# Performance work log

Hardware: AMD Instinct MI355X
Metric: run time of the kernel (lower is better)

Reference implementation:

```python
import jax, jax.numpy as jnp
import numpy as np

B, T, C = 4, 2048, 1024
H = 16
DH = C // H  # 64


def setup_inputs() -> dict:
    key = jax.random.key(0)
    ks = jax.random.split(key, 10)
    s_in = 1.0 / np.sqrt(C)
    x = jax.random.normal(ks[0], (B, T, C), dtype=jnp.float32)
    # stacked per-head projection weights: [H, C, DH]
    Wq = jax.random.normal(ks[1], (H, C, DH), dtype=jnp.float32) * s_in
    bq = jnp.zeros((H, DH), dtype=jnp.float32)
    Wk = jax.random.normal(ks[2], (H, C, DH), dtype=jnp.float32) * s_in
    bk = jnp.zeros((H, DH), dtype=jnp.float32)
    Wv = jax.random.normal(ks[3], (H, C, DH), dtype=jnp.float32) * s_in
    bv = jnp.zeros((H, DH), dtype=jnp.float32)
    Wo = jax.random.normal(ks[4], (C, C), dtype=jnp.float32) * s_in
    bo = jnp.zeros((C,), dtype=jnp.float32)
    return {"x": x, "Wq": Wq, "bq": bq, "Wk": Wk, "bk": bk,
            "Wv": Wv, "bv": bv, "Wo": Wo, "bo": bo}


def reference(x, Wq, bq, Wk, bk, Wv, bv, Wo, bo):
    # per-head projections: (B,T,C) x (H,C,DH) -> (B,H,T,DH)
    q = jnp.einsum('btc,hcd->bhtd', x, Wq) + bq[None, :, None, :]
    k = jnp.einsum('btc,hcd->bhtd', x, Wk) + bk[None, :, None, :]
    v = jnp.einsum('btc,hcd->bhtd', x, Wv) + bv[None, :, None, :]
    # scores scaled by C**-0.5 (C = full input embedding dim, as in source)
    scale = jnp.float32(C) ** -0.5
    scores = jnp.einsum('bhtd,bhsd->bhts', q, k) * scale  # (B,H,T,T)
    causal = jnp.tril(jnp.ones((T, T), dtype=bool))
    scores = jnp.where(causal, scores, -jnp.inf)
    attn = jax.nn.softmax(scores, axis=-1)
    out = jnp.einsum('bhts,bhsd->bhtd', attn, v)  # (B,H,T,DH)
    out = out.transpose(0, 2, 1, 3).reshape(B, T, C)  # concat heads
    return out @ Wo + bo
```

## Files before the change

### kernel.cpp

```cpp
#include <hip/hip_runtime.h>
#include <hip/hip_bf16.h>

#define TDIM 2048
#define BDIM 4
#define CDIM 1024
#define HDIM 16
#define DH   64

typedef __hip_bfloat16 bf16;
typedef __attribute__((ext_vector_type(8))) short bf16x8;
typedef __attribute__((ext_vector_type(4))) short bf16x4;
typedef __attribute__((ext_vector_type(4))) float f32x4;

__device__ __forceinline__ void async_ld16(const bf16* g, bf16* l) {
    __builtin_amdgcn_global_load_lds(
        (const __attribute__((address_space(1))) unsigned int*)g,
        (__attribute__((address_space(3))) unsigned int*)l, 16, 0, 0);
}

__device__ __forceinline__ unsigned short bf16bits(float x) {
    bf16 b = __float2bfloat16(x);
    return *(unsigned short*)&b;
}

__device__ __forceinline__ float fast_exp2(float x) {
#if __has_builtin(__builtin_amdgcn_exp2f)
    return __builtin_amdgcn_exp2f(x);
#else
    return exp2f(x);
#endif
}

__device__ __forceinline__ f32x4 mfma_16x16x16_bf16(bf16x4 a, bf16x4 b, f32x4 c) {
#if __has_builtin(__builtin_amdgcn_mfma_f32_16x16x16_bf16)
    return __builtin_amdgcn_mfma_f32_16x16x16_bf16(a, b, c, 0, 0, 0);
#elif __has_builtin(__builtin_amdgcn_mfma_f32_16x16x16bf16_1k)
    return __builtin_amdgcn_mfma_f32_16x16x16bf16_1k(a, b, c, 0, 0, 0);
#else
    asm volatile("v_mfma_f32_16x16x16_bf16 %0, %1, %2, %0"
                 : "+v"(c) : "v"(a), "v"(b));
    return c;
#endif
}

__global__ void convert_x4(const float4* __restrict__ src, ushort4* __restrict__ dst, int n4) {
    int i = blockIdx.x * blockDim.x + threadIdx.x;
    if (i >= n4) return;
    float4 v = src[i];
    ushort4 o;
    o.x = bf16bits(v.x); o.y = bf16bits(v.y);
    o.z = bf16bits(v.z); o.w = bf16bits(v.w);
    dst[i] = o;
}

__global__ void convert_biases(const float* __restrict__ b0, const float* __restrict__ b1,
                               const float* __restrict__ b2, const float* __restrict__ b3,
                               bf16* __restrict__ dst) {
    int i = blockIdx.x * blockDim.x + threadIdx.x;
    int which = i >> 10, j = i & 1023;
    const float* src = (which == 0) ? b0 : (which == 1) ? b1 : (which == 2) ? b2 : b3;
    dst[i] = __float2bfloat16(src[j]);
}

__global__ __launch_bounds__(256) void transpose_qkv_kernel(
    const float* __restrict__ Wq, const float* __restrict__ Wk, const float* __restrict__ Wv,
    bf16* __restrict__ WqT, bf16* __restrict__ WkT, bf16* __restrict__ WvT) {
    __shared__ float tile[64][65];
    const int which = blockIdx.z >> 4, h = blockIdx.z & 15;
    const float* W  = ((which == 0) ? Wq  : (which == 1) ? Wk  : Wv)  + (size_t)h * CDIM * DH;
    bf16*        WT = ((which == 0) ? WqT : (which == 1) ? WkT : WvT) + (size_t)h * CDIM * DH;
    const int c0 = blockIdx.x * 64;
    for (int it = 0; it < 16; it++) {
        int e = it * 256 + threadIdx.x;
        int r = e >> 6, col = e & 63;
        tile[r][col] = W[(size_t)(c0 + r) * DH + col];
    }
    __syncthreads();
    for (int it = 0; it < 16; it++) {
        int e = it * 256 + threadIdx.x;
        int r = e >> 6, col = e & 63;
        WT[(size_t)r * CDIM + c0 + col] = __float2bfloat16(tile[col][r]);
    }
}

__global__ __launch_bounds__(256) void transpose_wo_kernel(
    const float* __restrict__ W, bf16* __restrict__ WT) {
    __shared__ float tile[64][65];
    const int c0 = blockIdx.x * 64, d0 = blockIdx.y * 64;
    for (int it = 0; it < 16; it++) {
        int e = it * 256 + threadIdx.x;
        int r = e >> 6, col = e & 63;
        tile[r][col] = W[(size_t)(c0 + r) * CDIM + d0 + col];
    }
    __syncthreads();
    for (int it = 0; it < 16; it++) {
        int e = it * 256 + threadIdx.x;
        int r = e >> 6, col = e & 63;
        WT[(size_t)(d0 + r) * CDIM + c0 + col] = __float2bfloat16(tile[col][r]);
    }
}

__global__ __launch_bounds__(256) void transpose_v_kernel(
    const bf16* __restrict__ V, bf16* __restrict__ Vt) {
    __shared__ unsigned short tile[64][65];
    const int bh = blockIdx.y, t0 = blockIdx.x * 64;
    const unsigned short* Vp  = (const unsigned short*)V + ((size_t)bh * TDIM + t0) * DH;
    unsigned short*       Vtp = (unsigned short*)Vt + (size_t)bh * DH * TDIM;
    for (int it = 0; it < 16; it++) {
        int e = it * 256 + threadIdx.x;
        int r = e >> 6, c = e & 63;
        tile[r][c] = Vp[(size_t)r * DH + c];
    }
    __syncthreads();
    for (int it = 0; it < 16; it++) {
        int e = it * 256 + threadIdx.x;
        int r = e >> 6, c = e & 63;
        Vtp[(size_t)r * TDIM + t0 + c] = tile[c][r];
    }
}

__global__ __launch_bounds__(256) void proj_qkv_kernel(
    const bf16* __restrict__ X,
    const bf16* __restrict__ WqT, const bf16* __restrict__ WkT, const bf16* __restrict__ WvT,
    const bf16* __restrict__ bq,  const bf16* __restrict__ bk,  const bf16* __restrict__ bvv,
    bf16* __restrict__ Qo, bf16* __restrict__ Ko, bf16* __restrict__ Vo)
{
    const int lin  = blockIdx.x + (int)gridDim.x * (blockIdx.y + (int)gridDim.y * blockIdx.z);
    const int xcd  = lin & 7;
    const int s    = lin >> 3;
    const int mloc = s & 7;
    const int rest = s >> 3;
    const int nblk = rest & 7;
    const int z    = rest >> 3;

    const bf16* Bt   = (z == 0) ? WqT : (z == 1) ? WkT : WvT;
    const bf16* bias = (z == 0) ? bq  : (z == 1) ? bk  : bvv;

    __shared__ __align__(16) bf16 As[128 * 32];
    __shared__ __align__(16) bf16 Bs[128 * 32];

    const int tid  = threadIdx.x;
    const int lane = tid & 63;
    const int wave = tid >> 6;
    const int wr = wave >> 1, wc = wave & 1;
    const int l15 = lane & 15, quad = lane >> 4;

    const int blockM = (xcd * 8 + mloc) * 128;
    const int blockN = nblk * 128;

    f32x4 acc[4][4];
    for (int i = 0; i < 4; i++)
        for (int j = 0; j < 4; j++)
            acc[i][j] = (f32x4){0.f, 0.f, 0.f, 0.f};

    const int srow = lane >> 2, scol = (lane & 3) * 8;
    for (int k0 = 0; k0 < CDIM; k0 += 32) {
        for (int cc = 0; cc < 2; cc++) {
            int chunk = wave * 2 + cc;
            int row = chunk * 16 + srow;
            async_ld16(&X [(size_t)(blockM + row) * CDIM + k0 + scol], &As[chunk * 512]);
            async_ld16(&Bt[(size_t)(blockN + row) * CDIM + k0 + scol], &Bs[chunk * 512]);
        }
        __syncthreads();

        bf16x8 af[4], bfr[4];
        for (int mi = 0; mi < 4; mi++)
            af[mi] = *(const bf16x8*)&As[(wr * 64 + mi * 16 + l15) * 32 + quad * 8];
        for (int ni = 0; ni < 4; ni++)
            bfr[ni] = *(const bf16x8*)&Bs[(wc * 64 + ni * 16 + l15) * 32 + quad * 8];

        for (int mi = 0; mi < 4; mi++)
            for (int ni = 0; ni < 4; ni++)
                acc[mi][ni] = __builtin_amdgcn_mfma_f32_16x16x32_bf16(
                    af[mi], bfr[ni], acc[mi][ni], 0, 0, 0);
        __syncthreads();
    }

    for (int mi = 0; mi < 4; mi++) {
        int mbase = blockM + wr * 64 + mi * 16 + quad * 4;
        for (int ni = 0; ni < 4; ni++) {
            int n = blockN + wc * 64 + ni * 16 + l15;
            float bval = __bfloat162float(bias[n]);
            int h = n >> 6, d = n & 63;
            for (int r = 0; r < 4; r++) {
                int mm = mbase + r;
                int b = mm >> 11, t = mm & 2047;
                float val = acc[mi][ni][r] + bval;
                size_t idx = (((size_t)b * HDIM + h) * TDIM + t) * DH + d;
                if (z == 0)      Qo[idx] = __float2bfloat16(val * 0.045084439f);
                else if (z == 1) Ko[idx] = __float2bfloat16(val);
                else             Vo[idx] = __float2bfloat16(val);
            }
        }
    }
}

__global__ __launch_bounds__(256) void proj_out_kernel(
    const bf16* __restrict__ X, const bf16* __restrict__ Bt,
    const bf16* __restrict__ bias, float* __restrict__ Out)
{
    const int lin  = blockIdx.x + (int)gridDim.x * blockIdx.y;
    const int xcd  = lin & 7;
    const int s    = lin >> 3;
    const int mloc = s & 7;
    const int nblk = s >> 3;

    __shared__ __align__(16) bf16 As[128 * 32];
    __shared__ __align__(16) bf16 Bs[128 * 32];

    const int tid  = threadIdx.x;
    const int lane = tid & 63;
    const int wave = tid >> 6;
    const int wr = wave >> 1, wc = wave & 1;
    const int l15 = lane & 15, quad = lane >> 4;

    const int blockM = (xcd * 8 + mloc) * 128;
    const int blockN = nblk * 128;

    f32x4 acc[4][4];
    for (int i = 0; i < 4; i++)
        for (int j = 0; j < 4; j++)
            acc[i][j] = (f32x4){0.f, 0.f, 0.f, 0.f};

    const int srow = lane >> 2, scol = (lane & 3) * 8;
    for (int k0 = 0; k0 < CDIM; k0 += 32) {
        for (int cc = 0; cc < 2; cc++) {
            int chunk = wave * 2 + cc;
            int row = chunk * 16 + srow;
            async_ld16(&X [(size_t)(blockM + row) * CDIM + k0 + scol], &As[chunk * 512]);
            async_ld16(&Bt[(size_t)(blockN + row) * CDIM + k0 + scol], &Bs[chunk * 512]);
        }
        __syncthreads();

        bf16x8 af[4], bfr[4];
        for (int mi = 0; mi < 4; mi++)
            af[mi] = *(const bf16x8*)&As[(wr * 64 + mi * 16 + l15) * 32 + quad * 8];
        for (int ni = 0; ni < 4; ni++)
            bfr[ni] = *(const bf16x8*)&Bs[(wc * 64 + ni * 16 + l15) * 32 + quad * 8];

        for (int mi = 0; mi < 4; mi++)
            for (int ni = 0; ni < 4; ni++)
                acc[mi][ni] = __builtin_amdgcn_mfma_f32_16x16x32_bf16(
                    af[mi], bfr[ni], acc[mi][ni], 0, 0, 0);
        __syncthreads();
    }

    for (int mi = 0; mi < 4; mi++) {
        int mbase = blockM + wr * 64 + mi * 16 + quad * 4;
        for (int ni = 0; ni < 4; ni++) {
            int n = blockN + wc * 64 + ni * 16 + l15;
            float bval = __bfloat162float(bias[n]);
            for (int r = 0; r < 4; r++)
                Out[(size_t)(mbase + r) * CDIM + n] = acc[mi][ni][r] + bval;
        }
    }
}

__global__ __launch_bounds__(256, 4) void attn_kernel(
    const bf16* __restrict__ Q, const bf16* __restrict__ Kb,
    const bf16* __restrict__ Vt, bf16* __restrict__ Y)
{
    const int lin  = blockIdx.x + (int)gridDim.x * blockIdx.y;
    const int slot = lin >> 3;
    const int bh   = (lin & 7) * 8 + (slot >> 4);
    const int qT   = 15 - (slot & 15);
    const int qBase = qT * 128;
    const int tid  = threadIdx.x;
    const int lane = tid & 63, wave = tid >> 6;
    const int l15 = lane & 15, quad = lane >> 4;

    __shared__ __align__(16) bf16 smem[2 * 2 * 64 * 64];

    bf16x8 qf[2][2];
    for (int g = 0; g < 2; g++) {
        const size_t qrow = (size_t)bh * TDIM + qBase + g * 64 + wave * 16 + l15;
        qf[g][0] = *(const bf16x8*)&Q[qrow * DH + quad * 8];
        qf[g][1] = *(const bf16x8*)&Q[qrow * DH + 32 + quad * 8];
    }

    f32x4 o[2][4];
    for (int g = 0; g < 2; g++)
        for (int mt = 0; mt < 4; mt++)
            o[g][mt] = (f32x4){0.f, 0.f, 0.f, 0.f};
    float lsum[2] = {0.f, 0.f};

    const int srow = (wave << 4) + (lane >> 3);
    const int ssc  = (((lane & 7) ^ (lane >> 3)) << 3);
    const bf16* kSrc0 = Kb + ((size_t)bh * TDIM + srow) * DH + ssc;
    const bf16* vSrc0 = Vt + ((size_t)bh * DH + srow) * TDIM + ssc;

    const int swA   = l15 & 7;
    const int kcol0 = ((quad ^ swA) << 3);
    const int kcol1 = (((4 + quad) ^ swA) << 3);
    const int u2    = quad >> 1, intra = ((quad & 1) << 2);

    const int nkt  = 2 * qT + 2;
    const int qloc = wave * 16 + l15;

    bf16* kD0 = smem + (wave * 16) * 64;
    bf16* vD0 = smem + 4096 + (wave * 16) * 64;

#define STAGE(tile, buf)                                            \
    do {                                                            \
        const bf16* kS_ = kSrc0 + (size_t)(tile) * 64 * DH;         \
        const bf16* vS_ = vSrc0 + (size_t)(tile) * 64;              \
        bf16* kD_ = kD0 + (buf) * 8192;                             \
        bf16* vD_ = vD0 + (buf) * 8192;                             \
        async_ld16(kS_,            kD_);                            \
        async_ld16(kS_ + 8 * DH,   kD_ + 8 * 64);                   \
        async_ld16(vS_,            vD_);                            \
        async_ld16(vS_ + 8 * TDIM, vD_ + 8 * 64);                   \
    } while (0)

    STAGE(0, 0);
    __syncthreads();

    int cur = 0;
    for (int kt = 0; kt < nkt; kt++) {
        if (kt + 1 < nkt) STAGE(kt + 1, cur ^ 1);
        const bf16* Ks = smem + cur * 8192;
        const bf16* Vs = Ks + 4096;

        const int dg = kt - 2 * qT;
        for (int nt = 0; nt < 4; nt++) {
            bf16x8 kf0 = *(const bf16x8*)&Ks[(nt * 16 + l15) * 64 + kcol0];
            bf16x8 kf1 = *(const bf16x8*)&Ks[(nt * 16 + l15) * 64 + kcol1];
            bf16x4 vA[4];
            for (int mt = 0; mt < 4; mt++)
                vA[mt] = *(const bf16x4*)&Vs[(mt * 16 + l15) * 64 +
                                             (((nt * 2 + u2) ^ swA) << 3) + intra];

            for (int g = 0; g < 2; g++) {
                if (dg == 1 && g == 0) continue;
                f32x4 s = (f32x4){0.f, 0.f, 0.f, 0.f};
                s = __builtin_amdgcn_mfma_f32_16x16x32_bf16(kf0, qf[g][0], s, 0, 0, 0);
                s = __builtin_amdgcn_mfma_f32_16x16x32_bf16(kf1, qf[g][1], s, 0, 0, 0);

                const bool diag = (dg == g);
                bf16x4 pb;
                for (int r = 0; r < 4; r++) {
                    float pe = fast_exp2(s[r]);
                    if (diag && (nt * 16 + quad * 4 + r > qloc)) pe = 0.f;
                    lsum[g] += pe;
                    pb[r] = (short)bf16bits(pe);
                }
                for (int mt = 0; mt < 4; mt++)
                    o[g][mt] = mfma_16x16x16_bf16(vA[mt], pb, o[g][mt]);
            }
        }
        __syncthreads();
        cur ^= 1;
    }
#undef STAGE

    const int b = bh >> 4, h = bh & 15;
    unsigned short* sm = (unsigned short*)smem;
    for (int g = 0; g < 2; g++) {
        float v = lsum[g];
        v += __shfl_xor(v, 16, 64);
        v += __shfl_xor(v, 32, 64);
        const float inv = 1.0f / v;

        for (int mt = 0; mt < 4; mt++) {
            unsigned short pk[4];
            for (int r = 0; r < 4; r++) pk[r] = bf16bits(o[g][mt][r] * inv);
            *(ushort4*)&sm[(wave * 16 + l15) * 72 + mt * 16 + quad * 4] = *(ushort4*)pk;
        }
        const int qq = lane >> 2, part = lane & 3;
        const int t = qBase + g * 64 + wave * 16 + qq;
        uint4 c0 = *(const uint4*)&sm[(wave * 16 + qq) * 72 + part * 16];
        uint4 c1 = *(const uint4*)&sm[(wave * 16 + qq) * 72 + part * 16 + 8];
        *(uint4*)&Y[((size_t)b * TDIM + t) * CDIM + h * DH + part * 16]     = c0;
        *(uint4*)&Y[((size_t)b * TDIM + t) * CDIM + h * DH + part * 16 + 8] = c1;
    }
}

extern "C" void kernel_launch(void* const* d_in, const int* in_sizes, int n_in,
                              void* d_out, int out_size, void* d_ws, size_t ws_size,
                              hipStream_t stream) {
    (void)in_sizes; (void)n_in; (void)out_size; (void)ws_size;

    char* ws = (char*)d_ws;
    const size_t SZ_BHTD = (size_t)BDIM * HDIM * TDIM * DH * sizeof(bf16);
    const size_t SZ_W    = (size_t)HDIM * CDIM * DH * sizeof(bf16);
    bf16* Qb  = (bf16*)(ws);
    bf16* Kb  = (bf16*)(ws + SZ_BHTD);
    bf16* Vt  = (bf16*)(ws + 2 * SZ_BHTD);
    bf16* Y   = (bf16*)(ws + 3 * SZ_BHTD);
    bf16* WqT = (bf16*)(ws + 4 * SZ_BHTD);
    bf16* WkT = (bf16*)(ws + 4 * SZ_BHTD + SZ_W);
    bf16* WvT = (bf16*)(ws + 4 * SZ_BHTD + 2 * SZ_W);
    bf16* WoT = (bf16*)(ws + 4 * SZ_BHTD + 3 * SZ_W);
    bf16* xC  = (bf16*)(ws + 4 * SZ_BHTD + 4 * SZ_W);
    bf16* bqC = (bf16*)(ws + 5 * SZ_BHTD + 4 * SZ_W);
    bf16* bkC = bqC + 1024;
    bf16* bvC = bqC + 2048;
    bf16* boC = bqC + 3072;
    bf16* Vb  = (bf16*)d_out;

    const int nX4 = (BDIM * TDIM * CDIM) / 4;
    convert_x4<<<nX4 / 256, 256, 0, stream>>>((const float4*)d_in[0], (ushort4*)xC, nX4);
    convert_biases<<<16, 256, 0, stream>>>((const float*)d_in[2], (const float*)d_in[4],
                                           (const float*)d_in[6], (const float*)d_in[8], bqC);

    transpose_qkv_kernel<<<dim3(CDIM / 64, 1, 48), 256, 0, stream>>>(
        (const float*)d_in[1], (const float*)d_in[3], (const float*)d_in[5], WqT, WkT, WvT);
    transpose_wo_kernel<<<dim3(CDIM / 64, CDIM / 64), 256, 0, stream>>>(
        (const float*)d_in[7], WoT);

    dim3 gq(CDIM / 128, (BDIM * TDIM) / 128, 3);
    proj_qkv_kernel<<<gq, 256, 0, stream>>>(xC, WqT, WkT, WvT, bqC, bkC, bvC, Qb, Kb, Vb);

    transpose_v_kernel<<<dim3(TDIM / 64, BDIM * HDIM), 256, 0, stream>>>(Vb, Vt);

    attn_kernel<<<dim3(TDIM / 128, BDIM * HDIM), 256, 0, stream>>>(Qb, Kb, Vt, Y);

    proj_out_kernel<<<dim3(CDIM / 128, (BDIM * TDIM) / 128), 256, 0, stream>>>(
        Y, WoT, boC, (float*)d_out);
}
```

Baseline: 280.4 us.

## Double-buffer GEMM LDS tiles and write V transposed from projection epilogue

Both projection GEMMs now use two LDS buffers, so the async global-to-LDS load for the next K tile is issued before the MFMAs on the current tile. This overlaps memory latency with compute and drops one barrier per iteration. The QKV projection epilogue writes V directly in transposed [b,h,d,t] layout with 4-element packed stores, which removes the separate transpose_v kernel and its round trip through global memory. The cost is twice the shared memory per block, which may lower occupancy.

```diff
diff --git a/kernel.cpp b/kernel.cpp
--- a/kernel.cpp
+++ b/kernel.cpp
@@ -100,30 +100,11 @@
     }
 }
 
-__global__ __launch_bounds__(256) void transpose_v_kernel(
-    const bf16* __restrict__ V, bf16* __restrict__ Vt) {
-    __shared__ unsigned short tile[64][65];
-    const int bh = blockIdx.y, t0 = blockIdx.x * 64;
-    const unsigned short* Vp  = (const unsigned short*)V + ((size_t)bh * TDIM + t0) * DH;
-    unsigned short*       Vtp = (unsigned short*)Vt + (size_t)bh * DH * TDIM;
-    for (int it = 0; it < 16; it++) {
-        int e = it * 256 + threadIdx.x;
-        int r = e >> 6, c = e & 63;
-        tile[r][c] = Vp[(size_t)r * DH + c];
-    }
-    __syncthreads();
-    for (int it = 0; it < 16; it++) {
-        int e = it * 256 + threadIdx.x;
-        int r = e >> 6, c = e & 63;
-        Vtp[(size_t)r * TDIM + t0 + c] = tile[c][r];
-    }
-}
-
 __global__ __launch_bounds__(256) void proj_qkv_kernel(
     const bf16* __restrict__ X,
     const bf16* __restrict__ WqT, const bf16* __restrict__ WkT, const bf16* __restrict__ WvT,
     const bf16* __restrict__ bq,  const bf16* __restrict__ bk,  const bf16* __restrict__ bvv,
-    bf16* __restrict__ Qo, bf16* __restrict__ Ko, bf16* __restrict__ Vo)
+    bf16* __restrict__ Qo, bf16* __restrict__ Ko, bf16* __restrict__ Vt)
 {
     const int lin  = blockIdx.x + (int)gridDim.x * (blockIdx.y + (int)gridDim.y * blockIdx.z);
     const int xcd  = lin & 7;
@@ -136,8 +117,8 @@
     const bf16* Bt   = (z == 0) ? WqT : (z == 1) ? WkT : WvT;
     const bf16* bias = (z == 0) ? bq  : (z == 1) ? bk  : bvv;
 
-    __shared__ __align__(16) bf16 As[128 * 32];
-    __shared__ __align__(16) bf16 Bs[128 * 32];
+    __shared__ __align__(16) bf16 As[2 * 128 * 32];
+    __shared__ __align__(16) bf16 Bs[2 * 128 * 32];
 
     const int tid  = threadIdx.x;
     const int lane = tid & 63;
@@ -154,42 +135,60 @@
             acc[i][j] = (f32x4){0.f, 0.f, 0.f, 0.f};
 
     const int srow = lane >> 2, scol = (lane & 3) * 8;
-    for (int k0 = 0; k0 < CDIM; k0 += 32) {
-        for (int cc = 0; cc < 2; cc++) {
-            int chunk = wave * 2 + cc;
-            int row = chunk * 16 + srow;
-            async_ld16(&X [(size_t)(blockM + row) * CDIM + k0 + scol], &As[chunk * 512]);
-            async_ld16(&Bt[(size_t)(blockN + row) * CDIM + k0 + scol], &Bs[chunk * 512]);
-        }
-        __syncthreads();
-
+#define PSTAGE(k0, buf)                                                          \
+    do {                                                                         \
+        for (int cc = 0; cc < 2; cc++) {                                         \
+            int chunk = wave * 2 + cc;                                           \
+            int row = chunk * 16 + srow;                                         \
+            async_ld16(&X [(size_t)(blockM + row) * CDIM + (k0) + scol],         \
+                       &As[(buf) * 4096 + chunk * 512]);                         \
+            async_ld16(&Bt[(size_t)(blockN + row) * CDIM + (k0) + scol],         \
+                       &Bs[(buf) * 4096 + chunk * 512]);                         \
+        }                                                                        \
+    } while (0)
+
+    PSTAGE(0, 0);
+    __syncthreads();
+
+    int cur = 0;
+    for (int kt = 0; kt < 32; kt++) {
+        if (kt + 1 < 32) PSTAGE((kt + 1) * 32, cur ^ 1);
+
+        const bf16* Ap = As + cur * 4096;
+        const bf16* Bp = Bs + cur * 4096;
         bf16x8 af[4], bfr[4];
         for (int mi = 0; mi < 4; mi++)
-            af[mi] = *(const bf16x8*)&As[(wr * 64 + mi * 16 + l15) * 32 + quad * 8];
+            af[mi] = *(const bf16x8*)&Ap[(wr * 64 + mi * 16 + l15) * 32 + quad * 8];
         for (int ni = 0; ni < 4; ni++)
-            bfr[ni] = *(const bf16x8*)&Bs[(wc * 64 + ni * 16 + l15) * 32 + quad * 8];
+            bfr[ni] = *(const bf16x8*)&Bp[(wc * 64 + ni * 16 + l15) * 32 + quad * 8];
 
         for (int mi = 0; mi < 4; mi++)
             for (int ni = 0; ni < 4; ni++)
                 acc[mi][ni] = __builtin_amdgcn_mfma_f32_16x16x32_bf16(
                     af[mi], bfr[ni], acc[mi][ni], 0, 0, 0);
         __syncthreads();
-    }
+        cur ^= 1;
+    }
+#undef PSTAGE
 
     for (int mi = 0; mi < 4; mi++) {
         int mbase = blockM + wr * 64 + mi * 16 + quad * 4;
+        int b = mbase >> 11, t = mbase & 2047;
         for (int ni = 0; ni < 4; ni++) {
             int n = blockN + wc * 64 + ni * 16 + l15;
             float bval = __bfloat162float(bias[n]);
             int h = n >> 6, d = n & 63;
-            for (int r = 0; r < 4; r++) {
-                int mm = mbase + r;
-                int b = mm >> 11, t = mm & 2047;
-                float val = acc[mi][ni][r] + bval;
-                size_t idx = (((size_t)b * HDIM + h) * TDIM + t) * DH + d;
-                if (z == 0)      Qo[idx] = __float2bfloat16(val * 0.045084439f);
-                else if (z == 1) Ko[idx] = __float2bfloat16(val);
-                else             Vo[idx] = __float2bfloat16(val);
+            if (z == 2) {
+                unsigned short pk[4];
+                for (int r = 0; r < 4; r++) pk[r] = bf16bits(acc[mi][ni][r] + bval);
+                *(ushort4*)&Vt[(((size_t)b * HDIM + h) * DH + d) * TDIM + t] = *(ushort4*)pk;
+            } else {
+                for (int r = 0; r < 4; r++) {
+                    float val = acc[mi][ni][r] + bval;
+                    size_t idx = (((size_t)b * HDIM + h) * TDIM + (t + r)) * DH + d;
+                    if (z == 0) Qo[idx] = __float2bfloat16(val * 0.045084439f);
+                    else        Ko[idx] = __float2bfloat16(val);
+                }
             }
         }
     }
@@ -205,8 +204,8 @@
     const int mloc = s & 7;
     const int nblk = s >> 3;
 
-    __shared__ __align__(16) bf16 As[128 * 32];
-    __shared__ __align__(16) bf16 Bs[128 * 32];
+    __shared__ __align__(16) bf16 As[2 * 128 * 32];
+    __shared__ __align__(16) bf16 Bs[2 * 128 * 32];
 
     const int tid  = threadIdx.x;
     const int lane = tid & 63;
@@ -223,27 +222,41 @@
             acc[i][j] = (f32x4){0.f, 0.f, 0.f, 0.f};
 
     const int srow = lane >> 2, scol = (lane & 3) * 8;
-    for (int k0 = 0; k0 < CDIM; k0 += 32) {
-        for (int cc = 0; cc < 2; cc++) {
-            int chunk = wave * 2 + cc;
-            int row = chunk * 16 + srow;
-            async_ld16(&X [(size_t)(blockM + row) * CDIM + k0 + scol], &As[chunk * 512]);
-            async_ld16(&Bt[(size_t)(blockN + row) * CDIM + k0 + scol], &Bs[chunk * 512]);
-        }
-        __syncthreads();
-
+#define PSTAGE(k0, buf)                                                          \
+    do {                                                                         \
+        for (int cc = 0; cc < 2; cc++) {                                         \
+            int chunk = wave * 2 + cc;                                           \
+            int row = chunk * 16 + srow;                                         \
+            async_ld16(&X [(size_t)(blockM + row) * CDIM + (k0) + scol],         \
+                       &As[(buf) * 4096 + chunk * 512]);                         \
+            async_ld16(&Bt[(size_t)(blockN + row) * CDIM + (k0) + scol],         \
+                       &Bs[(buf) * 4096 + chunk * 512]);                         \
+        }                                                                        \
+    } while (0)
+
+    PSTAGE(0, 0);
+    __syncthreads();
+
+    int cur = 0;
+    for (int kt = 0; kt < 32; kt++) {
+        if (kt + 1 < 32) PSTAGE((kt + 1) * 32, cur ^ 1);
+
+        const bf16* Ap = As + cur * 4096;
+        const bf16* Bp = Bs + cur * 4096;
         bf16x8 af[4], bfr[4];
         for (int mi = 0; mi < 4; mi++)
-            af[mi] = *(const bf16x8*)&As[(wr * 64 + mi * 16 + l15) * 32 + quad * 8];
+            af[mi] = *(const bf16x8*)&Ap[(wr * 64 + mi * 16 + l15) * 32 + quad * 8];
         for (int ni = 0; ni < 4; ni++)
-            bfr[ni] = *(const bf16x8*)&Bs[(wc * 64 + ni * 16 + l15) * 32 + quad * 8];
+            bfr[ni] = *(const bf16x8*)&Bp[(wc * 64 + ni * 16 + l15) * 32 + quad * 8];
 
         for (int mi = 0; mi < 4; mi++)
             for (int ni = 0; ni < 4; ni++)
                 acc[mi][ni] = __builtin_amdgcn_mfma_f32_16x16x32_bf16(
                     af[mi], bfr[ni], acc[mi][ni], 0, 0, 0);
         __syncthreads();
-    }
+        cur ^= 1;
+    }
+#undef PSTAGE
 
     for (int mi = 0; mi < 4; mi++) {
         int mbase = blockM + wr * 64 + mi * 16 + quad * 4;
@@ -396,7 +409,6 @@
     bf16* bkC = bqC + 1024;
     bf16* bvC = bqC + 2048;
     bf16* boC = bqC + 3072;
-    bf16* Vb  = (bf16*)d_out;
 
     const int nX4 = (BDIM * TDIM * CDIM) / 4;
     convert_x4<<<nX4 / 256, 256, 0, stream>>>((const float4*)d_in[0], (ushort4*)xC, nX4);
@@ -409,9 +421,7 @@
         (const float*)d_in[7], WoT);
 
     dim3 gq(CDIM / 128, (BDIM * TDIM) / 128, 3);
-    proj_qkv_kernel<<<gq, 256, 0, stream>>>(xC, WqT, WkT, WvT, bqC, bkC, bvC, Qb, Kb, Vb);
-
-    transpose_v_kernel<<<dim3(TDIM / 64, BDIM * HDIM), 256, 0, stream>>>(Vb, Vt);
+    proj_qkv_kernel<<<gq, 256, 0, stream>>>(xC, WqT, WkT, WvT, bqC, bkC, bvC, Qb, Kb, Vt);
 
     attn_kernel<<<dim3(TDIM / 128, BDIM * HDIM), 256, 0, stream>>>(Qb, Kb, Vt, Y);
 
```

New measurement: 288.1 us. 1.03x slower.
